# Optimization experiments

Hardware: AMD Instinct MI355X
Metric: run time of the kernel (lower is better)

The kernel has to match this reference:

```python
import jax, jax.numpy as jnp
import numpy as np

N, C, D = 8192, 16, 5

def setup_inputs() -> dict:
    key = jax.random.key(0)
    k1, k2 = jax.random.split(key)
    U = jax.random.normal(k1, (N, C), dtype=jnp.float32)
    ref = jax.random.normal(k2, (N, D), dtype=jnp.float32)
    return {"U": U, "ref": ref}

def reference(U, ref):
    # Exact Gaussian bilateral filter that the permutohedral lattice approximates:
    # out_i = sum_j exp(-0.5 * ||ref_i - ref_j||^2) * U_j  -  U_i
    sq = jnp.sum(ref * ref, axis=-1)                      # [N]
    # squared pairwise distances via gram trick: ||ri||^2 + ||rj||^2 - 2 ri.rj
    d2 = sq[:, None] + sq[None, :] - 2.0 * (ref @ ref.T)  # [N, N]
    W = jnp.exp(-0.5 * jnp.maximum(d2, 0.0))              # [N, N] Gaussian kernel
    return W @ U - U                                      # [N, C]
```

## Files before the change

kernel.cpp:

```cpp
#include <hip/hip_runtime.h>


#define N_ROWS 8192
#define C_CH   16
#define D_DIM  5
#define TPB    256
#define NIB    (N_ROWS / TPB)

#if __has_builtin(__builtin_amdgcn_exp2f)
#define EXP2(x) __builtin_amdgcn_exp2f(x)
#else
#define EXP2(x) exp2f(x)
#endif

#define LOG2E 1.4426950408889634f

struct alignas(32) RefPack {
    float s[8];
};

__global__ __launch_bounds__(TPB) void lg_pre(const float* __restrict__ ref,
                                              RefPack* __restrict__ pack) {
    const int j = blockIdx.x * TPB + threadIdx.x;
    float v0 = ref[j * D_DIM + 0];
    float v1 = ref[j * D_DIM + 1];
    float v2 = ref[j * D_DIM + 2];
    float v3 = ref[j * D_DIM + 3];
    float v4 = ref[j * D_DIM + 4];
    float s = v0 * v0;
    s = fmaf(v1, v1, s); s = fmaf(v2, v2, s);
    s = fmaf(v3, v3, s); s = fmaf(v4, v4, s);
    RefPack p;
    p.s[0] = v0 * LOG2E; p.s[1] = v1 * LOG2E; p.s[2] = v2 * LOG2E;
    p.s[3] = v3 * LOG2E; p.s[4] = v4 * LOG2E;
    p.s[5] = -0.5f * LOG2E * s;
    p.s[6] = 0.0f; p.s[7] = 0.0f;
    pack[j] = p;
}

template <int NSEG>
__global__ __launch_bounds__(TPB) void lg_main(const float* __restrict__ U,
                                               const float* __restrict__ ref,
                                               const RefPack* __restrict__ pack,
                                               float* __restrict__ part) {
    constexpr int JPB = N_ROWS / NSEG;
    const int bid = blockIdx.x;
    const int ib  = bid % NIB;
    const int seg = bid / NIB;
    const int i   = ib * TPB + threadIdx.x;

    const float r0 = ref[i * D_DIM + 0];
    const float r1 = ref[i * D_DIM + 1];
    const float r2 = ref[i * D_DIM + 2];
    const float r3 = ref[i * D_DIM + 3];
    const float r4 = ref[i * D_DIM + 4];
    float ai = r0 * r0;
    ai = fmaf(r1, r1, ai); ai = fmaf(r2, r2, ai);
    ai = fmaf(r3, r3, ai); ai = fmaf(r4, r4, ai);
    ai = -0.5f * LOG2E * ai;

    float acc[C_CH];
#pragma unroll
    for (int c = 0; c < C_CH; ++c) acc[c] = 0.0f;

    const float4* __restrict__ U4 = reinterpret_cast<const float4*>(U);

    const int j0 = seg * JPB;
#pragma unroll 4
    for (int j = j0; j < j0 + JPB; ++j) {
        const RefPack rp = pack[j];

        float e = ai + rp.s[5];
        e = fmaf(r0, rp.s[0], e);
        e = fmaf(r1, rp.s[1], e);
        e = fmaf(r2, rp.s[2], e);
        e = fmaf(r3, rp.s[3], e);
        e = fmaf(r4, rp.s[4], e);
        const float w = EXP2(e);

        const float4 u0 = U4[j * 4 + 0];
        const float4 u1 = U4[j * 4 + 1];
        const float4 u2 = U4[j * 4 + 2];
        const float4 u3 = U4[j * 4 + 3];

        acc[0]  = fmaf(w, u0.x, acc[0]);   acc[1]  = fmaf(w, u0.y, acc[1]);
        acc[2]  = fmaf(w, u0.z, acc[2]);   acc[3]  = fmaf(w, u0.w, acc[3]);
        acc[4]  = fmaf(w, u1.x, acc[4]);   acc[5]  = fmaf(w, u1.y, acc[5]);
        acc[6]  = fmaf(w, u1.z, acc[6]);   acc[7]  = fmaf(w, u1.w, acc[7]);
        acc[8]  = fmaf(w, u2.x, acc[8]);   acc[9]  = fmaf(w, u2.y, acc[9]);
        acc[10] = fmaf(w, u2.z, acc[10]);  acc[11] = fmaf(w, u2.w, acc[11]);
        acc[12] = fmaf(w, u3.x, acc[12]);  acc[13] = fmaf(w, u3.y, acc[13]);
        acc[14] = fmaf(w, u3.z, acc[14]);  acc[15] = fmaf(w, u3.w, acc[15]);
    }

    float4* p4 = reinterpret_cast<float4*>(part + ((size_t)seg * N_ROWS + i) * C_CH);
    p4[0] = make_float4(acc[0], acc[1], acc[2], acc[3]);
    p4[1] = make_float4(acc[4], acc[5], acc[6], acc[7]);
    p4[2] = make_float4(acc[8], acc[9], acc[10], acc[11]);
    p4[3] = make_float4(acc[12], acc[13], acc[14], acc[15]);
}

template <int NSEG>
__global__ __launch_bounds__(TPB) void lg_reduce(const float* __restrict__ U,
                                                 const float* __restrict__ part,
                                                 float* __restrict__ out) {
    const int t = blockIdx.x * TPB + threadIdx.x;
    const float4 u = reinterpret_cast<const float4*>(U)[t];
    float4 s = make_float4(-u.x, -u.y, -u.z, -u.w);
    const float4* p = reinterpret_cast<const float4*>(part);
#pragma unroll 8
    for (int seg = 0; seg < NSEG; ++seg) {
        const float4 v = p[(size_t)seg * (N_ROWS * C_CH / 4) + t];
        s.x += v.x; s.y += v.y; s.z += v.z; s.w += v.w;
    }
    reinterpret_cast<float4*>(out)[t] = s;
}


__global__ __launch_bounds__(TPB) void lg_init(const float* __restrict__ U,
                                               float* __restrict__ out) {
    const int idx = blockIdx.x * TPB + threadIdx.x;
    if (idx < N_ROWS * C_CH) out[idx] = -U[idx];
}

__global__ __launch_bounds__(TPB) void lg_main_atomic(const float* __restrict__ U,
                                                      const float* __restrict__ ref,
                                                      float* __restrict__ out) {
    constexpr int NSEG = 32;
    constexpr int JPB  = N_ROWS / NSEG;
    const int bid = blockIdx.x;
    const int ib  = bid % NIB;
    const int seg = bid / NIB;
    const int i   = ib * TPB + threadIdx.x;

    const float r0 = ref[i * D_DIM + 0];
    const float r1 = ref[i * D_DIM + 1];
    const float r2 = ref[i * D_DIM + 2];
    const float r3 = ref[i * D_DIM + 3];
    const float r4 = ref[i * D_DIM + 4];

    float acc[C_CH];
#pragma unroll
    for (int c = 0; c < C_CH; ++c) acc[c] = 0.0f;

    const float4* __restrict__ U4 = reinterpret_cast<const float4*>(U);
    const int j0 = seg * JPB;
#pragma unroll 4
    for (int j = j0; j < j0 + JPB; ++j) {
        const float d0 = r0 - ref[j * D_DIM + 0];
        const float d1 = r1 - ref[j * D_DIM + 1];
        const float d2 = r2 - ref[j * D_DIM + 2];
        const float d3 = r3 - ref[j * D_DIM + 3];
        const float d4 = r4 - ref[j * D_DIM + 4];
        float dsq = d0 * d0;
        dsq = fmaf(d1, d1, dsq); dsq = fmaf(d2, d2, dsq);
        dsq = fmaf(d3, d3, dsq); dsq = fmaf(d4, d4, dsq);
        const float w = __expf(-0.5f * dsq);

        const float4 u0 = U4[j * 4 + 0];
        const float4 u1 = U4[j * 4 + 1];
        const float4 u2 = U4[j * 4 + 2];
        const float4 u3 = U4[j * 4 + 3];
        acc[0]  = fmaf(w, u0.x, acc[0]);   acc[1]  = fmaf(w, u0.y, acc[1]);
        acc[2]  = fmaf(w, u0.z, acc[2]);   acc[3]  = fmaf(w, u0.w, acc[3]);
        acc[4]  = fmaf(w, u1.x, acc[4]);   acc[5]  = fmaf(w, u1.y, acc[5]);
        acc[6]  = fmaf(w, u1.z, acc[6]);   acc[7]  = fmaf(w, u1.w, acc[7]);
        acc[8]  = fmaf(w, u2.x, acc[8]);   acc[9]  = fmaf(w, u2.y, acc[9]);
        acc[10] = fmaf(w, u2.z, acc[10]);  acc[11] = fmaf(w, u2.w, acc[11]);
        acc[12] = fmaf(w, u3.x, acc[12]);  acc[13] = fmaf(w, u3.y, acc[13]);
        acc[14] = fmaf(w, u3.z, acc[14]);  acc[15] = fmaf(w, u3.w, acc[15]);
    }

    float* o = out + (size_t)i * C_CH;
#pragma unroll
    for (int c = 0; c < C_CH; ++c) atomicAdd(&o[c], acc[c]);
}

extern "C" void kernel_launch(void* const* d_in, const int* in_sizes, int n_in,
                              void* d_out, int out_size, void* d_ws, size_t ws_size,
                              hipStream_t stream) {
    const float* U   = (const float*)d_in[0];
    const float* ref = (const float*)d_in[1];
    float* out       = (float*)d_out;

    const size_t pack_bytes = (size_t)N_ROWS * sizeof(RefPack);
    const size_t part_elems = [](int nseg) {
        return (size_t)nseg * N_ROWS * C_CH;
    }(1);

    const size_t need64 = pack_bytes + 64 * part_elems * sizeof(float);
    const size_t need32 = pack_bytes + 32 * part_elems * sizeof(float);

    if (ws_size >= need64) {
        RefPack* pack = (RefPack*)d_ws;
        float* part   = (float*)((char*)d_ws + pack_bytes);
        hipLaunchKernelGGL(lg_pre, dim3(N_ROWS / TPB), dim3(TPB), 0, stream, ref, pack);
        hipLaunchKernelGGL((lg_main<64>), dim3(NIB * 64), dim3(TPB), 0, stream,
                           U, ref, pack, part);
        hipLaunchKernelGGL((lg_reduce<64>), dim3(N_ROWS * C_CH / 4 / TPB), dim3(TPB),
                           0, stream, U, part, out);
    } else if (ws_size >= need32) {
        RefPack* pack = (RefPack*)d_ws;
        float* part   = (float*)((char*)d_ws + pack_bytes);
        hipLaunchKernelGGL(lg_pre, dim3(N_ROWS / TPB), dim3(TPB), 0, stream, ref, pack);
        hipLaunchKernelGGL((lg_main<32>), dim3(NIB * 32), dim3(TPB), 0, stream,
                           U, ref, pack, part);
        hipLaunchKernelGGL((lg_reduce<32>), dim3(N_ROWS * C_CH / 4 / TPB), dim3(TPB),
                           0, stream, U, part, out);
    } else {
        hipLaunchKernelGGL(lg_init, dim3((N_ROWS * C_CH + TPB - 1) / TPB), dim3(TPB),
                           0, stream, U, out);
        hipLaunchKernelGGL(lg_main_atomic, dim3(NIB * 32), dim3(TPB), 0, stream,
                           U, ref, out);
    }
}
```

Baseline: 119.3 us.

## Stage j-tile in LDS, compute two rows per thread, fuse ref prepacking

Removes the separate prepack kernel and has each block compute the scaled ref terms and load its U tile into shared memory. Each thread now handles two output rows, so every LDS-read U/ref value feeds twice as many FMAs. This targets repeated global/L1 loads of pack and U per row and one kernel launch. In exchange the grid is halved, register pressure doubles (32 accumulators), and each block adds a barrier plus redundant per-block prepack work.

```diff
diff --git a/kernel.cpp b/kernel.cpp
--- a/kernel.cpp
+++ b/kernel.cpp
@@ -5,7 +5,9 @@
 #define C_CH   16
 #define D_DIM  5
 #define TPB    256
-#define NIB    (N_ROWS / TPB)
+#define MI     2
+#define IPB    (TPB * MI)
+#define NIB    (N_ROWS / IPB)
 
 #if __has_builtin(__builtin_amdgcn_exp2f)
 #define EXP2(x) __builtin_amdgcn_exp2f(x)
@@ -15,89 +17,111 @@
 
 #define LOG2E 1.4426950408889634f
 
-struct alignas(32) RefPack {
-    float s[8];
-};
-
-__global__ __launch_bounds__(TPB) void lg_pre(const float* __restrict__ ref,
-                                              RefPack* __restrict__ pack) {
-    const int j = blockIdx.x * TPB + threadIdx.x;
-    float v0 = ref[j * D_DIM + 0];
-    float v1 = ref[j * D_DIM + 1];
-    float v2 = ref[j * D_DIM + 2];
-    float v3 = ref[j * D_DIM + 3];
-    float v4 = ref[j * D_DIM + 4];
-    float s = v0 * v0;
-    s = fmaf(v1, v1, s); s = fmaf(v2, v2, s);
-    s = fmaf(v3, v3, s); s = fmaf(v4, v4, s);
-    RefPack p;
-    p.s[0] = v0 * LOG2E; p.s[1] = v1 * LOG2E; p.s[2] = v2 * LOG2E;
-    p.s[3] = v3 * LOG2E; p.s[4] = v4 * LOG2E;
-    p.s[5] = -0.5f * LOG2E * s;
-    p.s[6] = 0.0f; p.s[7] = 0.0f;
-    pack[j] = p;
-}
-
 template <int NSEG>
 __global__ __launch_bounds__(TPB) void lg_main(const float* __restrict__ U,
                                                const float* __restrict__ ref,
-                                               const RefPack* __restrict__ pack,
                                                float* __restrict__ part) {
     constexpr int JPB = N_ROWS / NSEG;
+
+    __shared__ float sj[JPB][8];
+    __shared__ float su[JPB][16];
+
     const int bid = blockIdx.x;
     const int ib  = bid % NIB;
     const int seg = bid / NIB;
-    const int i   = ib * TPB + threadIdx.x;
-
-    const float r0 = ref[i * D_DIM + 0];
-    const float r1 = ref[i * D_DIM + 1];
-    const float r2 = ref[i * D_DIM + 2];
-    const float r3 = ref[i * D_DIM + 3];
-    const float r4 = ref[i * D_DIM + 4];
-    float ai = r0 * r0;
-    ai = fmaf(r1, r1, ai); ai = fmaf(r2, r2, ai);
-    ai = fmaf(r3, r3, ai); ai = fmaf(r4, r4, ai);
-    ai = -0.5f * LOG2E * ai;
-
-    float acc[C_CH];
+    const int tid = threadIdx.x;
+    const int j0  = seg * JPB;
+
+    const int i0 = ib * IPB + tid;
+    const int i1 = i0 + TPB;
+    const float r00 = ref[i0 * D_DIM + 0], r10 = ref[i1 * D_DIM + 0];
+    const float r01 = ref[i0 * D_DIM + 1], r11 = ref[i1 * D_DIM + 1];
+    const float r02 = ref[i0 * D_DIM + 2], r12 = ref[i1 * D_DIM + 2];
+    const float r03 = ref[i0 * D_DIM + 3], r13 = ref[i1 * D_DIM + 3];
+    const float r04 = ref[i0 * D_DIM + 4], r14 = ref[i1 * D_DIM + 4];
+
+    for (int jj = tid; jj < JPB; jj += TPB) {
+        const int j = j0 + jj;
+        const float v0 = ref[j * D_DIM + 0];
+        const float v1 = ref[j * D_DIM + 1];
+        const float v2 = ref[j * D_DIM + 2];
+        const float v3 = ref[j * D_DIM + 3];
+        const float v4 = ref[j * D_DIM + 4];
+        float s = v0 * v0;
+        s = fmaf(v1, v1, s); s = fmaf(v2, v2, s);
+        s = fmaf(v3, v3, s); s = fmaf(v4, v4, s);
+        sj[jj][0] = v0 * LOG2E; sj[jj][1] = v1 * LOG2E;
+        sj[jj][2] = v2 * LOG2E; sj[jj][3] = v3 * LOG2E;
+        sj[jj][4] = v4 * LOG2E; sj[jj][5] = -0.5f * LOG2E * s;
+        sj[jj][6] = 0.0f;       sj[jj][7] = 0.0f;
+    }
+    {
+        const float4* __restrict__ U4 = reinterpret_cast<const float4*>(U);
+        float4* su4 = reinterpret_cast<float4*>(&su[0][0]);
+        for (int idx = tid; idx < JPB * 4; idx += TPB)
+            su4[idx] = U4[(size_t)j0 * 4 + idx];
+    }
+    __syncthreads();
+
+    float a0 = r00 * r00, a1 = r10 * r10;
+    a0 = fmaf(r01, r01, a0); a1 = fmaf(r11, r11, a1);
+    a0 = fmaf(r02, r02, a0); a1 = fmaf(r12, r12, a1);
+    a0 = fmaf(r03, r03, a0); a1 = fmaf(r13, r13, a1);
+    a0 = fmaf(r04, r04, a0); a1 = fmaf(r14, r14, a1);
+    a0 *= -0.5f * LOG2E;     a1 *= -0.5f * LOG2E;
+
+    float acc0[C_CH], acc1[C_CH];
 #pragma unroll
-    for (int c = 0; c < C_CH; ++c) acc[c] = 0.0f;
-
-    const float4* __restrict__ U4 = reinterpret_cast<const float4*>(U);
-
-    const int j0 = seg * JPB;
-#pragma unroll 4
-    for (int j = j0; j < j0 + JPB; ++j) {
-        const RefPack rp = pack[j];
-
-        float e = ai + rp.s[5];
-        e = fmaf(r0, rp.s[0], e);
-        e = fmaf(r1, rp.s[1], e);
-        e = fmaf(r2, rp.s[2], e);
-        e = fmaf(r3, rp.s[3], e);
-        e = fmaf(r4, rp.s[4], e);
-        const float w = EXP2(e);
-
-        const float4 u0 = U4[j * 4 + 0];
-        const float4 u1 = U4[j * 4 + 1];
-        const float4 u2 = U4[j * 4 + 2];
-        const float4 u3 = U4[j * 4 + 3];
-
-        acc[0]  = fmaf(w, u0.x, acc[0]);   acc[1]  = fmaf(w, u0.y, acc[1]);
-        acc[2]  = fmaf(w, u0.z, acc[2]);   acc[3]  = fmaf(w, u0.w, acc[3]);
-        acc[4]  = fmaf(w, u1.x, acc[4]);   acc[5]  = fmaf(w, u1.y, acc[5]);
-        acc[6]  = fmaf(w, u1.z, acc[6]);   acc[7]  = fmaf(w, u1.w, acc[7]);
-        acc[8]  = fmaf(w, u2.x, acc[8]);   acc[9]  = fmaf(w, u2.y, acc[9]);
-        acc[10] = fmaf(w, u2.z, acc[10]);  acc[11] = fmaf(w, u2.w, acc[11]);
-        acc[12] = fmaf(w, u3.x, acc[12]);  acc[13] = fmaf(w, u3.y, acc[13]);
-        acc[14] = fmaf(w, u3.z, acc[14]);  acc[15] = fmaf(w, u3.w, acc[15]);
-    }
-
-    float4* p4 = reinterpret_cast<float4*>(part + ((size_t)seg * N_ROWS + i) * C_CH);
-    p4[0] = make_float4(acc[0], acc[1], acc[2], acc[3]);
-    p4[1] = make_float4(acc[4], acc[5], acc[6], acc[7]);
-    p4[2] = make_float4(acc[8], acc[9], acc[10], acc[11]);
-    p4[3] = make_float4(acc[12], acc[13], acc[14], acc[15]);
+    for (int c = 0; c < C_CH; ++c) { acc0[c] = 0.0f; acc1[c] = 0.0f; }
+
+#pragma unroll 8
+    for (int jj = 0; jj < JPB; ++jj) {
+        const float4 sA = *reinterpret_cast<const float4*>(&sj[jj][0]);
+        const float2 sB = *reinterpret_cast<const float2*>(&sj[jj][4]);
+
+        float e0 = a0 + sB.y;
+        float e1 = a1 + sB.y;
+        e0 = fmaf(r00, sA.x, e0);  e1 = fmaf(r10, sA.x, e1);
+        e0 = fmaf(r01, sA.y, e0);  e1 = fmaf(r11, sA.y, e1);
+        e0 = fmaf(r02, sA.z, e0);  e1 = fmaf(r12, sA.z, e1);
+        e0 = fmaf(r03, sA.w, e0);  e1 = fmaf(r13, sA.w, e1);
+        e0 = fmaf(r04, sB.x, e0);  e1 = fmaf(r14, sB.x, e1);
+        const float w0 = EXP2(e0);
+        const float w1 = EXP2(e1);
+
+        const float4 u0 = *reinterpret_cast<const float4*>(&su[jj][0]);
+        const float4 u1 = *reinterpret_cast<const float4*>(&su[jj][4]);
+        const float4 u2 = *reinterpret_cast<const float4*>(&su[jj][8]);
+        const float4 u3 = *reinterpret_cast<const float4*>(&su[jj][12]);
+
+        acc0[0]  = fmaf(w0, u0.x, acc0[0]);   acc1[0]  = fmaf(w1, u0.x, acc1[0]);
+        acc0[1]  = fmaf(w0, u0.y, acc0[1]);   acc1[1]  = fmaf(w1, u0.y, acc1[1]);
+        acc0[2]  = fmaf(w0, u0.z, acc0[2]);   acc1[2]  = fmaf(w1, u0.z, acc1[2]);
+        acc0[3]  = fmaf(w0, u0.w, acc0[3]);   acc1[3]  = fmaf(w1, u0.w, acc1[3]);
+        acc0[4]  = fmaf(w0, u1.x, acc0[4]);   acc1[4]  = fmaf(w1, u1.x, acc1[4]);
+        acc0[5]  = fmaf(w0, u1.y, acc0[5]);   acc1[5]  = fmaf(w1, u1.y, acc1[5]);
+        acc0[6]  = fmaf(w0, u1.z, acc0[6]);   acc1[6]  = fmaf(w1, u1.z, acc1[6]);
+        acc0[7]  = fmaf(w0, u1.w, acc0[7]);   acc1[7]  = fmaf(w1, u1.w, acc1[7]);
+        acc0[8]  = fmaf(w0, u2.x, acc0[8]);   acc1[8]  = fmaf(w1, u2.x, acc1[8]);
+        acc0[9]  = fmaf(w0, u2.y, acc0[9]);   acc1[9]  = fmaf(w1, u2.y, acc1[9]);
+        acc0[10] = fmaf(w0, u2.z, acc0[10]);  acc1[10] = fmaf(w1, u2.z, acc1[10]);
+        acc0[11] = fmaf(w0, u2.w, acc0[11]);  acc1[11] = fmaf(w1, u2.w, acc1[11]);
+        acc0[12] = fmaf(w0, u3.x, acc0[12]);  acc1[12] = fmaf(w1, u3.x, acc1[12]);
+        acc0[13] = fmaf(w0, u3.y, acc0[13]);  acc1[13] = fmaf(w1, u3.y, acc1[13]);
+        acc0[14] = fmaf(w0, u3.z, acc0[14]);  acc1[14] = fmaf(w1, u3.z, acc1[14]);
+        acc0[15] = fmaf(w0, u3.w, acc0[15]);  acc1[15] = fmaf(w1, u3.w, acc1[15]);
+    }
+
+    float4* p0 = reinterpret_cast<float4*>(part + ((size_t)seg * N_ROWS + i0) * C_CH);
+    float4* p1 = reinterpret_cast<float4*>(part + ((size_t)seg * N_ROWS + i1) * C_CH);
+    p0[0] = make_float4(acc0[0],  acc0[1],  acc0[2],  acc0[3]);
+    p0[1] = make_float4(acc0[4],  acc0[5],  acc0[6],  acc0[7]);
+    p0[2] = make_float4(acc0[8],  acc0[9],  acc0[10], acc0[11]);
+    p0[3] = make_float4(acc0[12], acc0[13], acc0[14], acc0[15]);
+    p1[0] = make_float4(acc1[0],  acc1[1],  acc1[2],  acc1[3]);
+    p1[1] = make_float4(acc1[4],  acc1[5],  acc1[6],  acc1[7]);
+    p1[2] = make_float4(acc1[8],  acc1[9],  acc1[10], acc1[11]);
+    p1[3] = make_float4(acc1[12], acc1[13], acc1[14], acc1[15]);
 }
 
 template <int NSEG>
@@ -128,9 +152,10 @@
                                                       float* __restrict__ out) {
     constexpr int NSEG = 32;
     constexpr int JPB  = N_ROWS / NSEG;
+    constexpr int NIB1 = N_ROWS / TPB;
     const int bid = blockIdx.x;
-    const int ib  = bid % NIB;
-    const int seg = bid / NIB;
+    const int ib  = bid % NIB1;
+    const int seg = bid / NIB1;
     const int i   = ib * TPB + threadIdx.x;
 
     const float r0 = ref[i * D_DIM + 0];
@@ -183,34 +208,26 @@
     const float* ref = (const float*)d_in[1];
     float* out       = (float*)d_out;
 
-    const size_t pack_bytes = (size_t)N_ROWS * sizeof(RefPack);
-    const size_t part_elems = [](int nseg) {
-        return (size_t)nseg * N_ROWS * C_CH;
-    }(1);
-
-    const size_t need64 = pack_bytes + 64 * part_elems * sizeof(float);
-    const size_t need32 = pack_bytes + 32 * part_elems * sizeof(float);
+    const size_t seg_bytes = (size_t)N_ROWS * C_CH * sizeof(float);
+    const size_t need64 = 64 * seg_bytes;
+    const size_t need32 = 32 * seg_bytes;
 
     if (ws_size >= need64) {
-        RefPack* pack = (RefPack*)d_ws;
-        float* part   = (float*)((char*)d_ws + pack_bytes);
-        hipLaunchKernelGGL(lg_pre, dim3(N_ROWS / TPB), dim3(TPB), 0, stream, ref, pack);
+        float* part = (float*)d_ws;
         hipLaunchKernelGGL((lg_main<64>), dim3(NIB * 64), dim3(TPB), 0, stream,
-                           U, ref, pack, part);
+                           U, ref, part);
         hipLaunchKernelGGL((lg_reduce<64>), dim3(N_ROWS * C_CH / 4 / TPB), dim3(TPB),
                            0, stream, U, part, out);
     } else if (ws_size >= need32) {
-        RefPack* pack = (RefPack*)d_ws;
-        float* part   = (float*)((char*)d_ws + pack_bytes);
-        hipLaunchKernelGGL(lg_pre, dim3(N_ROWS / TPB), dim3(TPB), 0, stream, ref, pack);
+        float* part = (float*)d_ws;
         hipLaunchKernelGGL((lg_main<32>), dim3(NIB * 32), dim3(TPB), 0, stream,
-                           U, ref, pack, part);
+                           U, ref, part);
         hipLaunchKernelGGL((lg_reduce<32>), dim3(N_ROWS * C_CH / 4 / TPB), dim3(TPB),
                            0, stream, U, part, out);
     } else {
         hipLaunchKernelGGL(lg_init, dim3((N_ROWS * C_CH + TPB - 1) / TPB), dim3(TPB),
                            0, stream, U, out);
-        hipLaunchKernelGGL(lg_main_atomic, dim3(NIB * 32), dim3(TPB), 0, stream,
-                           U, ref, out);
-    }
-}
+        hipLaunchKernelGGL(lg_main_atomic, dim3((N_ROWS / TPB) * 32), dim3(TPB),
+                           0, stream, U, ref, out);
+    }
+}
```

Result: faster. 104.7 us (-12.2%).
